# Kernel optimization log

Hardware: AMD Instinct MI355X
Metric: run time of the kernel (lower is better)

## Reference

```python
import jax, jax.numpy as jnp
import numpy as np

INPUT_DIM = 128
DEPTH = 6
HIDDEN = 64
NUM_INNER = 2 ** DEPTH - 1  # 63
NUM_LEAVES = 2 ** DEPTH     # 64


def setup_inputs() -> dict:
    key = jax.random.key(0)
    ks = jax.random.split(key, 6)
    x = jax.random.normal(ks[0], (65536, INPUT_DIM), dtype=jnp.float32)
    s1 = 1.0 / np.sqrt(INPUT_DIM)
    s2 = 1.0 / np.sqrt(HIDDEN)
    W1 = jax.random.uniform(ks[1], (NUM_INNER, INPUT_DIM, HIDDEN), minval=-s1, maxval=s1, dtype=jnp.float32)
    b1 = jax.random.uniform(ks[2], (NUM_INNER, HIDDEN), minval=-s1, maxval=s1, dtype=jnp.float32)
    W2 = jax.random.uniform(ks[3], (NUM_INNER, HIDDEN), minval=-s2, maxval=s2, dtype=jnp.float32)
    b2 = jax.random.uniform(ks[4], (NUM_INNER,), minval=-s2, maxval=s2, dtype=jnp.float32)
    leaf = jax.random.normal(ks[5], (NUM_LEAVES, 1), dtype=jnp.float32)
    return {"x": x, "W1": W1, "b1": b1, "W2": W2, "b2": b2, "leaf": leaf}


def reference(x, W1, b1, W2, b2, leaf):
    # All inner-node MLPs as one batched GEMM pair: [B, N] node probabilities
    h = jax.nn.relu(jnp.einsum('bi,nih->bnh', x, W1) + b1)      # [B, N, H]
    probs = jax.nn.sigmoid(jnp.einsum('bnh,nh->bn', h, W2) + b2)  # [B, N]

    # Original code walks node_idx = 2*node_idx+1 unconditionally, so the chain
    # of used node indices is 2^k - 1 for k = 0..depth-1.
    chain = jnp.array([2 ** k - 1 for k in range(DEPTH)], dtype=jnp.int32)
    p_chain = probs[:, chain]  # [B, D]

    # Bit k (LSB first) of leaf index selects p (bit=1) vs 1-p (bit=0)
    leaves = np.arange(NUM_LEAVES)
    bits = jnp.asarray(((leaves[:, None] >> np.arange(DEPTH)[None, :]) & 1).astype(np.float32))  # [L, D]

    # path_probs[b, l] = prod_k ( bits[l,k]*p + (1-bits[l,k])*(1-p) )
    factors = bits[None, :, :] * p_chain[:, None, :] + (1.0 - bits[None, :, :]) * (1.0 - p_chain[:, None, :])  # [B, L, D]
    path_probs = jnp.prod(factors, axis=-1)  # [B, L]

    return (path_probs @ leaf)[:, 0]  # [B]
```

## Files before the change

kernel.cpp:

```cpp
#include <hip/hip_runtime.h>

typedef __attribute__((ext_vector_type(4))) float f32x4;
typedef __attribute__((ext_vector_type(8))) short bf16x8;
typedef __attribute__((ext_vector_type(4))) unsigned int u32x4;

#define IDIM    128
#define HID     64
#define TDEPTH  6
#define MTILE   64
#define NWAVES  6
#define BLOCK   (NWAVES * 64)
#define T_TILES 2

__device__ __forceinline__ unsigned short f2bf(float f) {
    unsigned int u = __builtin_bit_cast(unsigned int, f);
    unsigned int r = (u + 0x7FFFu + ((u >> 16) & 1u)) >> 16;
    return (unsigned short)r;
}

__device__ __forceinline__ unsigned int f2bf_pk(float f0, float f1) {
    unsigned int u0 = __builtin_bit_cast(unsigned int, f0);
    unsigned int u1 = __builtin_bit_cast(unsigned int, f1);
    unsigned int t0 = u0 + 0x7FFFu + ((u0 >> 16) & 1u);
    unsigned int t1 = u1 + 0x7FFFu + ((u1 >> 16) & 1u);
    return (t1 & 0xFFFF0000u) | (t0 >> 16);
}

__global__ __launch_bounds__(BLOCK, 3)
void sdt_kernel(const float* __restrict__ x, const float* __restrict__ W1,
                const float* __restrict__ b1, const float* __restrict__ W2,
                const float* __restrict__ b2, const float* __restrict__ leaf,
                float* __restrict__ out) {
    __shared__ unsigned short xs[MTILE][IDIM + 8];
    __shared__ float p_lds[TDEPTH][MTILE];
    __shared__ float pp[2][4][MTILE];
    __shared__ float leaf_lds[64];

    const int tid   = threadIdx.x;
    const int tile0 = blockIdx.x * T_TILES;

    const int wave = tid >> 6;
    const int lane = tid & 63;
    const int node = (1 << wave) - 1;
    const int lcol = lane & 15;
    const int lq   = lane >> 4;

    if (tid < 64) leaf_lds[tid] = leaf[tid];

    const float4* xv = reinterpret_cast<const float4*>(x);

    {
        const float4* xt = xv + (size_t)tile0 * (MTILE * IDIM / 4);
        for (int f = tid; f < MTILE * (IDIM / 4); f += BLOCK) {
            int row = f >> 5, c4 = f & 31;
            float4 v = xt[f];
            unsigned long long pk =
                (unsigned long long)f2bf(v.x) |
                ((unsigned long long)f2bf(v.y) << 16) |
                ((unsigned long long)f2bf(v.z) << 32) |
                ((unsigned long long)f2bf(v.w) << 48);
            *reinterpret_cast<unsigned long long*>(&xs[row][c4 * 4]) = pk;
        }
    }

    bf16x8 bfrag[4][4];
    {
        const float* wsrc = W1 + (size_t)node * IDIM * HID + lcol;
        #pragma unroll
        for (int ks = 0; ks < 4; ks++) {
            const int k0 = ks * 32 + lq * 8;
            #pragma unroll
            for (int ct = 0; ct < 4; ct++) {
                const float* wc = wsrc + (size_t)k0 * HID + ct * 16;
                u32x4 pk;
                #pragma unroll
                for (int jp = 0; jp < 4; jp++)
                    pk[jp] = f2bf_pk(wc[(2 * jp) * HID], wc[(2 * jp + 1) * HID]);
                bfrag[ks][ct] = __builtin_bit_cast(bf16x8, pk);
            }
        }
    }

    float b1v[4], w2v[4];
    #pragma unroll
    for (int ct = 0; ct < 4; ct++) {
        int col = ct * 16 + lcol;
        b1v[ct] = b1[node * HID + col];
        w2v[ct] = W2[node * HID + col];
    }
    const float bias2 = b2[node];

    __syncthreads();

    for (int t = 0; t < T_TILES; ++t) {
        f32x4 acc[4][4];
        #pragma unroll
        for (int rt = 0; rt < 4; rt++)
            #pragma unroll
            for (int ct = 0; ct < 4; ct++)
                acc[rt][ct] = (f32x4){0.f, 0.f, 0.f, 0.f};
        #pragma unroll
        for (int ks = 0; ks < 4; ks++) {
            #pragma unroll
            for (int rt = 0; rt < 4; rt++) {
                bf16x8 afrag = *reinterpret_cast<const bf16x8*>(
                    &xs[rt * 16 + lcol][ks * 32 + lq * 8]);
                #pragma unroll
                for (int ct = 0; ct < 4; ct++)
                    acc[rt][ct] = __builtin_amdgcn_mfma_f32_16x16x32_bf16(
                        afrag, bfrag[ks][ct], acc[rt][ct], 0, 0, 0);
            }
        }

        #pragma unroll
        for (int rt = 0; rt < 4; rt++) {
            #pragma unroll
            for (int r = 0; r < 4; r++) {
                float s = 0.f;
                #pragma unroll
                for (int ct = 0; ct < 4; ct++) {
                    float v = acc[rt][ct][r] + b1v[ct];
                    v = v > 0.f ? v : 0.f;
                    s += v * w2v[ct];
                }
                #pragma unroll
                for (int d = 1; d < 16; d <<= 1)
                    s += __shfl_xor(s, d, 64);
                float p = 1.f / (1.f + __expf(-(s + bias2)));
                if (lcol == 0)
                    p_lds[wave][rt * 16 + lq * 4 + r] = p;
            }
        }
        __syncthreads();

        if (t > 0 && tid < MTILE) {
            const float* q = &pp[(t - 1) & 1][0][0];
            out[(size_t)(tile0 + t - 1) * MTILE + tid] =
                (q[0 * MTILE + tid] + q[1 * MTILE + tid]) +
                (q[2 * MTILE + tid] + q[3 * MTILE + tid]);
        }

        if (tid < 4 * MTILE) {
            int row = tid & (MTILE - 1);
            int ch  = tid >> 6;
            float q0 = p_lds[0][row];
            float q1 = p_lds[1][row];
            float q2 = p_lds[2][row];
            float q3 = p_lds[3][row];
            float p4 = p_lds[4][row];
            float p5 = p_lds[5][row];
            float f4 = (ch & 1) ? p4 : 1.f - p4;
            float f5 = (ch & 2) ? p5 : 1.f - p5;
            const float* lf = leaf_lds + ch * 16;
            float tt[8];
            #pragma unroll
            for (int j = 0; j < 8; j++) {
                float a = lf[2 * j], b = lf[2 * j + 1];
                tt[j] = a + q0 * (b - a);
            }
            #pragma unroll
            for (int j = 0; j < 4; j++) tt[j] = tt[2 * j] + q1 * (tt[2 * j + 1] - tt[2 * j]);
            #pragma unroll
            for (int j = 0; j < 2; j++) tt[j] = tt[2 * j] + q2 * (tt[2 * j + 1] - tt[2 * j]);
            float s = tt[0] + q3 * (tt[1] - tt[0]);
            pp[t & 1][ch][row] = f4 * f5 * s;
        }

        if (t + 1 < T_TILES) {
            const float4* xt = xv + (size_t)(tile0 + t + 1) * (MTILE * IDIM / 4);
            for (int f = tid; f < MTILE * (IDIM / 4); f += BLOCK) {
                int row = f >> 5, c4 = f & 31;
                float4 v = xt[f];
                unsigned long long pk =
                    (unsigned long long)f2bf(v.x) |
                    ((unsigned long long)f2bf(v.y) << 16) |
                    ((unsigned long long)f2bf(v.z) << 32) |
                    ((unsigned long long)f2bf(v.w) << 48);
                *reinterpret_cast<unsigned long long*>(&xs[row][c4 * 4]) = pk;
            }
        }
        __syncthreads();
    }

    if (tid < MTILE) {
        const float* q = &pp[(T_TILES - 1) & 1][0][0];
        out[(size_t)(tile0 + T_TILES - 1) * MTILE + tid] =
            (q[0 * MTILE + tid] + q[1 * MTILE + tid]) +
            (q[2 * MTILE + tid] + q[3 * MTILE + tid]);
    }
}

extern "C" void kernel_launch(void* const* d_in, const int* in_sizes, int n_in,
                              void* d_out, int out_size, void* d_ws, size_t ws_size,
                              hipStream_t stream) {
    const float* x    = (const float*)d_in[0];
    const float* W1   = (const float*)d_in[1];
    const float* b1   = (const float*)d_in[2];
    const float* W2   = (const float*)d_in[3];
    const float* b2   = (const float*)d_in[4];
    const float* leaf = (const float*)d_in[5];
    float* out = (float*)d_out;

    const int Bn = in_sizes[0] / IDIM;
    const int nblocks = Bn / (MTILE * T_TILES);

    (void)d_ws; (void)ws_size;
    sdt_kernel<<<nblocks, BLOCK, 0, stream>>>(x, W1, b1, W2, b2, leaf, out);
}
```

Before: 113.9 us.

## Pre-pack W1 bf16 MFMA fragments in workspace and reload per k-step

```diff
diff --git a/kernel.cpp b/kernel.cpp
--- a/kernel.cpp
+++ b/kernel.cpp
@@ -11,6 +11,7 @@
 #define NWAVES  6
 #define BLOCK   (NWAVES * 64)
 #define T_TILES 2
+#define WFRAG_ELEMS (6 * 4 * 4 * 512)
 
 __device__ __forceinline__ unsigned short f2bf(float f) {
     unsigned int u = __builtin_bit_cast(unsigned int, f);
@@ -26,11 +27,26 @@
     return (t1 & 0xFFFF0000u) | (t0 >> 16);
 }
 
+__global__ void prep_wfrag(const float* __restrict__ W1, unsigned short* __restrict__ wfrag) {
+    int idx = blockIdx.x * 256 + threadIdx.x;
+    if (idx >= WFRAG_ELEMS) return;
+    int j    = idx & 7;
+    int lane = (idx >> 3) & 63;
+    int ct   = (idx >> 9) & 3;
+    int ks   = (idx >> 11) & 3;
+    int nd   = idx >> 13;
+    int node = (1 << nd) - 1;
+    int k    = ks * 32 + (lane >> 4) * 8 + j;
+    int col  = ct * 16 + (lane & 15);
+    wfrag[idx] = f2bf(W1[(node * IDIM + k) * HID + col]);
+}
+
+template <bool USE_WS>
 __global__ __launch_bounds__(BLOCK, 3)
 void sdt_kernel(const float* __restrict__ x, const float* __restrict__ W1,
                 const float* __restrict__ b1, const float* __restrict__ W2,
                 const float* __restrict__ b2, const float* __restrict__ leaf,
-                float* __restrict__ out) {
+                const unsigned short* __restrict__ wfrag, float* __restrict__ out) {
     __shared__ unsigned short xs[MTILE][IDIM + 8];
     __shared__ float p_lds[TDEPTH][MTILE];
     __shared__ float pp[2][4][MTILE];
@@ -63,24 +79,6 @@
         }
     }
 
-    bf16x8 bfrag[4][4];
-    {
-        const float* wsrc = W1 + (size_t)node * IDIM * HID + lcol;
-        #pragma unroll
-        for (int ks = 0; ks < 4; ks++) {
-            const int k0 = ks * 32 + lq * 8;
-            #pragma unroll
-            for (int ct = 0; ct < 4; ct++) {
-                const float* wc = wsrc + (size_t)k0 * HID + ct * 16;
-                u32x4 pk;
-                #pragma unroll
-                for (int jp = 0; jp < 4; jp++)
-                    pk[jp] = f2bf_pk(wc[(2 * jp) * HID], wc[(2 * jp + 1) * HID]);
-                bfrag[ks][ct] = __builtin_bit_cast(bf16x8, pk);
-            }
-        }
-    }
-
     float b1v[4], w2v[4];
     #pragma unroll
     for (int ct = 0; ct < 4; ct++) {
@@ -101,6 +99,25 @@
                 acc[rt][ct] = (f32x4){0.f, 0.f, 0.f, 0.f};
         #pragma unroll
         for (int ks = 0; ks < 4; ks++) {
+            bf16x8 bfrag[4];
+            if (USE_WS) {
+                #pragma unroll
+                for (int ct = 0; ct < 4; ct++)
+                    bfrag[ct] = *reinterpret_cast<const bf16x8*>(
+                        wfrag + (((wave * 4 + ks) * 4 + ct) * 512 + lane * 8));
+            } else {
+                const float* wsrc = W1 + (size_t)node * IDIM * HID + lcol;
+                const int k0 = ks * 32 + lq * 8;
+                #pragma unroll
+                for (int ct = 0; ct < 4; ct++) {
+                    const float* wc = wsrc + (size_t)k0 * HID + ct * 16;
+                    u32x4 pk;
+                    #pragma unroll
+                    for (int jp = 0; jp < 4; jp++)
+                        pk[jp] = f2bf_pk(wc[(2 * jp) * HID], wc[(2 * jp + 1) * HID]);
+                    bfrag[ct] = __builtin_bit_cast(bf16x8, pk);
+                }
+            }
             #pragma unroll
             for (int rt = 0; rt < 4; rt++) {
                 bf16x8 afrag = *reinterpret_cast<const bf16x8*>(
@@ -108,7 +125,7 @@
                 #pragma unroll
                 for (int ct = 0; ct < 4; ct++)
                     acc[rt][ct] = __builtin_amdgcn_mfma_f32_16x16x32_bf16(
-                        afrag, bfrag[ks][ct], acc[rt][ct], 0, 0, 0);
+                        afrag, bfrag[ct], acc[rt][ct], 0, 0, 0);
             }
         }
 
@@ -204,6 +221,11 @@
     const int Bn = in_sizes[0] / IDIM;
     const int nblocks = Bn / (MTILE * T_TILES);
 
-    (void)d_ws; (void)ws_size;
-    sdt_kernel<<<nblocks, BLOCK, 0, stream>>>(x, W1, b1, W2, b2, leaf, out);
-}
+    if (ws_size >= (size_t)WFRAG_ELEMS * sizeof(unsigned short)) {
+        unsigned short* wfrag = (unsigned short*)d_ws;
+        prep_wfrag<<<(WFRAG_ELEMS + 255) / 256, 256, 0, stream>>>(W1, wfrag);
+        sdt_kernel<true><<<nblocks, BLOCK, 0, stream>>>(x, W1, b1, W2, b2, leaf, wfrag, out);
+    } else {
+        sdt_kernel<false><<<nblocks, BLOCK, 0, stream>>>(x, W1, b1, W2, b2, leaf, nullptr, out);
+    }
+}
```

Measured after the change: 115.0 us. About the same (+0.9%).
